# Optimization experiments

Hardware: AMD Instinct MI355X
Metric: run time of the kernel (lower is better)

The kernel has to match this reference:

```python
import jax, jax.numpy as jnp
import numpy as np

N = 50000
E = 1600000
R = 4
D_IN = 128
D_OUT = 128


def setup_inputs() -> dict:
    key = jax.random.key(0)
    ks = jax.random.split(key, 7)
    x = jax.random.normal(ks[0], (N, D_IN), dtype=jnp.float32)
    vals = jax.random.normal(ks[1], (R, E), dtype=jnp.float32) * (1.0 / 32.0)
    weight = jax.random.normal(ks[2], (D_IN, D_OUT), dtype=jnp.float32) * (1.0 / np.sqrt(D_IN))
    filt = jax.random.uniform(ks[3], (R * N, 1), dtype=jnp.float32, minval=0.9, maxval=1.1)
    bias = jnp.zeros((D_OUT,), dtype=jnp.float32)
    rows = jax.random.randint(ks[4], (R, E), 0, N, dtype=jnp.int32)
    cols = jax.random.randint(ks[5], (R, E), 0, N, dtype=jnp.int32)
    return {"x": x, "vals": vals, "weight": weight, "filt": filt,
            "bias": bias, "rows": rows, "cols": cols}


def _spmm(rows, cols, vals, h, n):
    # sparse [n,n] @ dense [n,d] via gather + segment_sum
    return jax.ops.segment_sum(vals[:, None] * h[cols], rows, num_segments=n)


def reference(x, vals, weight, filt, bias, rows, cols):
    n = x.shape[0]
    h = x @ weight                                    # [N, out]
    # cat(d_list, dim=0) @ h  ->  stack of D_i @ h, i.e. [R, N, out]
    y = jax.vmap(lambda r, c, v: _spmm(r, c, v, h, n))(rows, cols, vals)
    y = filt.reshape(rows.shape[0], n, 1) * y         # elementwise wavelet filter
    # cat(d_list, dim=1) @ y  ->  sum_i D_i @ y_i
    out = jax.vmap(lambda r, c, v, yy: _spmm(r, c, v, yy, n))(rows, cols, vals, y).sum(axis=0)
    return out + bias
```

## Files before the change

kernel.cpp:

```cpp
#include <hip/hip_runtime.h>

#define N_NODES 50000
#define N_EDGES 1600000
#define R_WAV 4
#define D 128
#define NB 391
#define CHUNK 4096
#define NPBLK ((N_EDGES + CHUNK - 1) / CHUNK)
#define MAXB 4800
#define RP_STRIDE 50016

typedef unsigned int u32;
typedef unsigned short u16;

static __device__ inline u16 f2bf(float f) {
    u32 u = __float_as_uint(f);
    u = (u + 0x7FFFu + ((u >> 16) & 1u)) >> 16;
    return (u16)u;
}
static __device__ inline float bf_lo(u32 u) { return __uint_as_float(u << 16); }
static __device__ inline float bf_hi(u32 u) { return __uint_as_float(u & 0xFFFF0000u); }

__global__ __launch_bounds__(128) void gemm_xw(const float* __restrict__ x,
                                               const float* __restrict__ W,
                                               u16* __restrict__ h) {
    const int j = threadIdx.x;
    const int row0 = blockIdx.x * 16;
    const float* xr = x + (size_t)row0 * D;
    float acc[16];
#pragma unroll
    for (int r = 0; r < 16; ++r) acc[r] = 0.f;
#pragma unroll 4
    for (int k = 0; k < 128; ++k) {
        const float w = W[k * D + j];
#pragma unroll
        for (int r = 0; r < 16; ++r) acc[r] += xr[r * D + k] * w;
    }
#pragma unroll
    for (int r = 0; r < 16; ++r) h[(size_t)(row0 + r) * D + j] = f2bf(acc[r]);
}

__global__ __launch_bounds__(256) void bucket_hist_all(const int* __restrict__ rows_all,
                                                       int* __restrict__ hist) {
    __shared__ int lh[NB];
    const int r = blockIdx.y;
    const int* rows = rows_all + (size_t)r * N_EDGES;
    const int tid = threadIdx.x;
    for (int i = tid; i < NB; i += 256) lh[i] = 0;
    __syncthreads();
    const int e0 = blockIdx.x * CHUNK;
    const int e1 = min(e0 + CHUNK, N_EDGES);
    for (int i = e0 + tid; i < e1; i += 256) atomicAdd(&lh[rows[i] >> 7], 1);
    __syncthreads();
    int* hc = hist + ((size_t)r * NPBLK + blockIdx.x) * NB;
    for (int i = tid; i < NB; i += 256) hc[i] = lh[i];
}

__global__ __launch_bounds__(512) void chunk_scan(const int* __restrict__ hist,
                                                  int* __restrict__ chunkpre,
                                                  int* __restrict__ cnt) {
    __shared__ int sa[512], sb[512];
    const int b = blockIdx.x;
    const int r = blockIdx.y;
    const int tid = threadIdx.x;
    const int v = (tid < NPBLK) ? hist[((size_t)r * NPBLK + tid) * NB + b] : 0;
    sa[tid] = v;
    int* cur = sa;
    int* nxt = sb;
    for (int d = 1; d < 512; d <<= 1) {
        __syncthreads();
        int t = cur[tid];
        if (tid >= d) t += cur[tid - d];
        nxt[tid] = t;
        int* tmp = cur; cur = nxt; nxt = tmp;
    }
    __syncthreads();
    const int excl = cur[tid] - v;
    if (tid < NPBLK) chunkpre[((size_t)r * NPBLK + tid) * NB + b] = excl;
    if (tid == NPBLK - 1) cnt[r * NB + b] = excl + v;
}

__global__ __launch_bounds__(512) void scan_buckets_all(const int* __restrict__ cnt4,
                                                        int* __restrict__ bptr4) {
    __shared__ int sa[512], sb[512];
    const int r = blockIdx.x;
    const int* cnt = cnt4 + r * NB;
    int* bptr = bptr4 + r * (NB + 1);
    const int tid = threadIdx.x;
    const int v = (tid < NB) ? cnt[tid] : 0;
    sa[tid] = v;
    int* cur = sa;
    int* nxt = sb;
    for (int d = 1; d < 512; d <<= 1) {
        __syncthreads();
        int t = cur[tid];
        if (tid >= d) t += cur[tid - d];
        nxt[tid] = t;
        int* tmp = cur; cur = nxt; nxt = tmp;
    }
    __syncthreads();
    const int excl = cur[tid] - v;
    if (tid <= NB) bptr[tid] = excl;
}

__global__ __launch_bounds__(256) void partition_kernel(const int* __restrict__ rows,
                                                        const int* __restrict__ cols,
                                                        const float* __restrict__ vals,
                                                        const int* __restrict__ bptr_all,
                                                        const int* __restrict__ chunkpre,
                                                        const int* __restrict__ hist,
                                                        u32* __restrict__ cvA,
                                                        u16* __restrict__ rowloc) {
    const int r = blockIdx.y;
    rows   += (size_t)r * N_EDGES;
    cols   += (size_t)r * N_EDGES;
    vals   += (size_t)r * N_EDGES;
    cvA    += (size_t)r * N_EDGES;
    rowloc += (size_t)r * N_EDGES;
    const int* bptr = bptr_all + r * (NB + 1);
    const int* hc   = hist     + ((size_t)r * NPBLK + blockIdx.x) * NB;
    const int* cp   = chunkpre + ((size_t)r * NPBLK + blockIdx.x) * NB;
    __shared__ int lh[NB], lptr[NB], lcur[NB], lbase[NB];
    __shared__ int sa[256], sb[256];
    __shared__ u32 st_cv[CHUNK];
    __shared__ u16 st_rl[CHUNK];
    const int tid = threadIdx.x;
    for (int i = tid; i < NB; i += 256) lh[i] = hc[i];
    __syncthreads();
    const int e0 = blockIdx.x * CHUNK;
    const int e1 = min(e0 + CHUNK, N_EDGES);
    const int cnt = e1 - e0;
    const int p0 = (2 * tid < NB) ? lh[2 * tid] : 0;
    const int p1 = (2 * tid + 1 < NB) ? lh[2 * tid + 1] : 0;
    sa[tid] = p0 + p1;
    int* cur = sa;
    int* nxt = sb;
    for (int d = 1; d < 256; d <<= 1) {
        __syncthreads();
        int t = cur[tid];
        if (tid >= d) t += cur[tid - d];
        nxt[tid] = t;
        int* tmp = cur; cur = nxt; nxt = tmp;
    }
    __syncthreads();
    const int pe = cur[tid] - (p0 + p1);
    if (2 * tid < NB)     { lptr[2 * tid] = pe;           lcur[2 * tid] = pe; }
    if (2 * tid + 1 < NB) { lptr[2 * tid + 1] = pe + p0;  lcur[2 * tid + 1] = pe + p0; }
    __syncthreads();
    for (int i = e0 + tid; i < e1; i += 256) {
        const int row = rows[i];
        const int b = row >> 7;
        const int pos = atomicAdd(&lcur[b], 1);
        st_cv[pos] = ((u32)f2bf(vals[i]) << 16) | ((u32)cols[i] & 0xFFFFu);
        st_rl[pos] = (u16)row;
    }
    for (int b = tid; b < NB; b += 256) lbase[b] = bptr[b] + cp[b] - lptr[b];
    __syncthreads();
    for (int i = tid; i < cnt; i += 256) {
        const u16 rl = st_rl[i];
        const int b = (int)rl >> 7;
        const int o = lbase[b] + i;
        cvA[o] = st_cv[i];
        rowloc[o] = rl;
    }
}

__global__ __launch_bounds__(256) void bucket_csr(const int* __restrict__ bptr_all,
                                                  const u32* __restrict__ cvA,
                                                  const u16* __restrict__ rowloc,
                                                  u32* __restrict__ cv4,
                                                  int* __restrict__ row_ptr) {
    const int r = blockIdx.y;
    const int* bptr = bptr_all + r * (NB + 1);
    cvA     += (size_t)r * N_EDGES;
    rowloc  += (size_t)r * N_EDGES;
    cv4     += (size_t)r * N_EDGES;
    row_ptr += r * RP_STRIDE;
    __shared__ int lh[128], lexcl[128], lcur[128];
    __shared__ u32 st[MAXB];
    const int b = blockIdx.x;
    const int s = bptr[b], e1 = bptr[b + 1];
    const int cnt = e1 - s;
    const int tid = threadIdx.x;
    if (tid < 128) lh[tid] = 0;
    __syncthreads();
    for (int i = s + tid; i < e1; i += 256)
        atomicAdd(&lh[(int)rowloc[i] & 127], 1);
    __syncthreads();
    if (tid < 64) {
        const int p0 = lh[2 * tid], p1 = lh[2 * tid + 1];
        int ssum = p0 + p1;
#pragma unroll
        for (int d = 1; d < 64; d <<= 1) {
            const int t = __shfl_up(ssum, d, 64);
            if (tid >= d) ssum += t;
        }
        const int pe = ssum - (p0 + p1);
        lexcl[2 * tid] = pe;          lcur[2 * tid] = pe;
        lexcl[2 * tid + 1] = pe + p0; lcur[2 * tid + 1] = pe + p0;
    }
    __syncthreads();
    for (int i = s + tid; i < e1; i += 256) {
        const int lr = (int)rowloc[i] & 127;
        const int pos = atomicAdd(&lcur[lr], 1);
        if (pos < MAXB) st[pos] = cvA[i];
    }
    __syncthreads();
    const int wb = (cnt < MAXB) ? cnt : MAXB;
    for (int i = tid; i < wb; i += 256) cv4[s + i] = st[i];
    if (tid < 128) {
        const int row = (b << 7) + tid;
        if (row < N_NODES) row_ptr[row] = s + lexcl[tid];
    }
    if (blockIdx.x == 0 && tid == 0) row_ptr[N_NODES] = N_EDGES;
}

__global__ __launch_bounds__(256) void spmm1(const int* __restrict__ row_ptr,
                                             const u32* __restrict__ cvp,
                                             const u32* __restrict__ h2,
                                             const float* __restrict__ filt,
                                             u32* __restrict__ y2) {
    const int r = blockIdx.y;
    row_ptr += r * RP_STRIDE;
    cvp     += (size_t)r * N_EDGES;
    filt    += (size_t)r * N_NODES;
    y2      += (size_t)r * (N_NODES * 64);
    const int row = __builtin_amdgcn_readfirstlane(blockIdx.x * 4 + (threadIdx.x >> 6));
    const int lane = threadIdx.x & 63;
    const int half = lane >> 5;
    const int l = lane & 31;
    int e = row_ptr[row];
    const int end = row_ptr[row + 1];
    float a0 = 0.f, a1 = 0.f, a2 = 0.f, a3 = 0.f;
    float b0 = 0.f, b1 = 0.f, b2 = 0.f, b3 = 0.f;
    for (; e + 16 <= end; e += 16) {
        u32 c[16];
#pragma unroll
        for (int i = 0; i < 16; ++i) c[i] = cvp[e + i];
        const u32 u0 = half ? c[1] : c[0];
        const u32 u1 = half ? c[3] : c[2];
        const u32 u2 = half ? c[5] : c[4];
        const u32 u3 = half ? c[7] : c[6];
        const u32 u4 = half ? c[9] : c[8];
        const u32 u5 = half ? c[11] : c[10];
        const u32 u6 = half ? c[13] : c[12];
        const u32 u7 = half ? c[15] : c[14];
        const uint2 g0 = *(const uint2*)(h2 + (u0 & 0xFFFFu) * 64 + 2 * l);
        const uint2 g1 = *(const uint2*)(h2 + (u1 & 0xFFFFu) * 64 + 2 * l);
        const uint2 g2 = *(const uint2*)(h2 + (u2 & 0xFFFFu) * 64 + 2 * l);
        const uint2 g3 = *(const uint2*)(h2 + (u3 & 0xFFFFu) * 64 + 2 * l);
        const uint2 g4 = *(const uint2*)(h2 + (u4 & 0xFFFFu) * 64 + 2 * l);
        const uint2 g5 = *(const uint2*)(h2 + (u5 & 0xFFFFu) * 64 + 2 * l);
        const uint2 g6 = *(const uint2*)(h2 + (u6 & 0xFFFFu) * 64 + 2 * l);
        const uint2 g7 = *(const uint2*)(h2 + (u7 & 0xFFFFu) * 64 + 2 * l);
        const float v0 = __uint_as_float(u0 & 0xFFFF0000u);
        const float v1 = __uint_as_float(u1 & 0xFFFF0000u);
        const float v2 = __uint_as_float(u2 & 0xFFFF0000u);
        const float v3 = __uint_as_float(u3 & 0xFFFF0000u);
        const float v4 = __uint_as_float(u4 & 0xFFFF0000u);
        const float v5 = __uint_as_float(u5 & 0xFFFF0000u);
        const float v6 = __uint_as_float(u6 & 0xFFFF0000u);
        const float v7 = __uint_as_float(u7 & 0xFFFF0000u);
        a0 += v0 * bf_lo(g0.x); a1 += v0 * bf_hi(g0.x);
        a2 += v0 * bf_lo(g0.y); a3 += v0 * bf_hi(g0.y);
        b0 += v1 * bf_lo(g1.x); b1 += v1 * bf_hi(g1.x);
        b2 += v1 * bf_lo(g1.y); b3 += v1 * bf_hi(g1.y);
        a0 += v2 * bf_lo(g2.x); a1 += v2 * bf_hi(g2.x);
        a2 += v2 * bf_lo(g2.y); a3 += v2 * bf_hi(g2.y);
        b0 += v3 * bf_lo(g3.x); b1 += v3 * bf_hi(g3.x);
        b2 += v3 * bf_lo(g3.y); b3 += v3 * bf_hi(g3.y);
        a0 += v4 * bf_lo(g4.x); a1 += v4 * bf_hi(g4.x);
        a2 += v4 * bf_lo(g4.y); a3 += v4 * bf_hi(g4.y);
        b0 += v5 * bf_lo(g5.x); b1 += v5 * bf_hi(g5.x);
        b2 += v5 * bf_lo(g5.y); b3 += v5 * bf_hi(g5.y);
        a0 += v6 * bf_lo(g6.x); a1 += v6 * bf_hi(g6.x);
        a2 += v6 * bf_lo(g6.y); a3 += v6 * bf_hi(g6.y);
        b0 += v7 * bf_lo(g7.x); b1 += v7 * bf_hi(g7.x);
        b2 += v7 * bf_lo(g7.y); b3 += v7 * bf_hi(g7.y);
    }
    for (; e + 8 <= end; e += 8) {
        const u32 c0 = cvp[e], c1 = cvp[e + 1], c2 = cvp[e + 2], c3 = cvp[e + 3];
        const u32 c4 = cvp[e + 4], c5 = cvp[e + 5], c6 = cvp[e + 6], c7 = cvp[e + 7];
        const u32 uA = half ? c1 : c0;
        const u32 uB = half ? c3 : c2;
        const u32 uC = half ? c5 : c4;
        const u32 uD = half ? c7 : c6;
        const uint2 gA = *(const uint2*)(h2 + (uA & 0xFFFFu) * 64 + 2 * l);
        const uint2 gB = *(const uint2*)(h2 + (uB & 0xFFFFu) * 64 + 2 * l);
        const uint2 gC = *(const uint2*)(h2 + (uC & 0xFFFFu) * 64 + 2 * l);
        const uint2 gD = *(const uint2*)(h2 + (uD & 0xFFFFu) * 64 + 2 * l);
        const float vA = __uint_as_float(uA & 0xFFFF0000u);
        const float vB = __uint_as_float(uB & 0xFFFF0000u);
        const float vC = __uint_as_float(uC & 0xFFFF0000u);
        const float vD = __uint_as_float(uD & 0xFFFF0000u);
        a0 += vA * bf_lo(gA.x); a1 += vA * bf_hi(gA.x);
        a2 += vA * bf_lo(gA.y); a3 += vA * bf_hi(gA.y);
        b0 += vB * bf_lo(gB.x); b1 += vB * bf_hi(gB.x);
        b2 += vB * bf_lo(gB.y); b3 += vB * bf_hi(gB.y);
        a0 += vC * bf_lo(gC.x); a1 += vC * bf_hi(gC.x);
        a2 += vC * bf_lo(gC.y); a3 += vC * bf_hi(gC.y);
        b0 += vD * bf_lo(gD.x); b1 += vD * bf_hi(gD.x);
        b2 += vD * bf_lo(gD.y); b3 += vD * bf_hi(gD.y);
    }
    for (; e < end; e += 2) {
        const u32 c0 = cvp[e];
        const u32 c1 = (e + 1 < end) ? cvp[e + 1] : 0u;
        const u32 uA = half ? c1 : c0;
        const uint2 gA = *(const uint2*)(h2 + (uA & 0xFFFFu) * 64 + 2 * l);
        const float vA = __uint_as_float(uA & 0xFFFF0000u);
        a0 += vA * bf_lo(gA.x); a1 += vA * bf_hi(gA.x);
        a2 += vA * bf_lo(gA.y); a3 += vA * bf_hi(gA.y);
    }
    a0 += b0; a1 += b1; a2 += b2; a3 += b3;
    a0 += __shfl_xor(a0, 32, 64);
    a1 += __shfl_xor(a1, 32, 64);
    a2 += __shfl_xor(a2, 32, 64);
    a3 += __shfl_xor(a3, 32, 64);
    const float f = filt[row];
    if (half == 0) {
        uint2 o;
        o.x = (u32)f2bf(f * a0) | ((u32)f2bf(f * a1) << 16);
        o.y = (u32)f2bf(f * a2) | ((u32)f2bf(f * a3) << 16);
        *(uint2*)(y2 + (size_t)row * 64 + 2 * l) = o;
    }
}

template <bool FIRST>
__global__ __launch_bounds__(256) void spmm2(const int* __restrict__ row_ptr,
                                             const u32* __restrict__ cvp,
                                             const u32* __restrict__ y2,
                                             const float* __restrict__ bias,
                                             float* __restrict__ out) {
    const int row = __builtin_amdgcn_readfirstlane(blockIdx.x * 4 + (threadIdx.x >> 6));
    const int lane = threadIdx.x & 63;
    const int half = lane >> 5;
    const int l = lane & 31;
    int e = row_ptr[row];
    const int end = row_ptr[row + 1];
    float a0 = 0.f, a1 = 0.f, a2 = 0.f, a3 = 0.f;
    float b0 = 0.f, b1 = 0.f, b2 = 0.f, b3 = 0.f;
    for (; e + 16 <= end; e += 16) {
        u32 c[16];
#pragma unroll
        for (int i = 0; i < 16; ++i) c[i] = cvp[e + i];
        const u32 u0 = half ? c[1] : c[0];
        const u32 u1 = half ? c[3] : c[2];
        const u32 u2 = half ? c[5] : c[4];
        const u32 u3 = half ? c[7] : c[6];
        const u32 u4 = half ? c[9] : c[8];
        const u32 u5 = half ? c[11] : c[10];
        const u32 u6 = half ? c[13] : c[12];
        const u32 u7 = half ? c[15] : c[14];
        const uint2 g0 = *(const uint2*)(y2 + (u0 & 0xFFFFu) * 64 + 2 * l);
        const uint2 g1 = *(const uint2*)(y2 + (u1 & 0xFFFFu) * 64 + 2 * l);
        const uint2 g2 = *(const uint2*)(y2 + (u2 & 0xFFFFu) * 64 + 2 * l);
        const uint2 g3 = *(const uint2*)(y2 + (u3 & 0xFFFFu) * 64 + 2 * l);
        const uint2 g4 = *(const uint2*)(y2 + (u4 & 0xFFFFu) * 64 + 2 * l);
        const uint2 g5 = *(const uint2*)(y2 + (u5 & 0xFFFFu) * 64 + 2 * l);
        const uint2 g6 = *(const uint2*)(y2 + (u6 & 0xFFFFu) * 64 + 2 * l);
        const uint2 g7 = *(const uint2*)(y2 + (u7 & 0xFFFFu) * 64 + 2 * l);
        const float v0 = __uint_as_float(u0 & 0xFFFF0000u);
        const float v1 = __uint_as_float(u1 & 0xFFFF0000u);
        const float v2 = __uint_as_float(u2 & 0xFFFF0000u);
        const float v3 = __uint_as_float(u3 & 0xFFFF0000u);
        const float v4 = __uint_as_float(u4 & 0xFFFF0000u);
        const float v5 = __uint_as_float(u5 & 0xFFFF0000u);
        const float v6 = __uint_as_float(u6 & 0xFFFF0000u);
        const float v7 = __uint_as_float(u7 & 0xFFFF0000u);
        a0 += v0 * bf_lo(g0.x); a1 += v0 * bf_hi(g0.x);
        a2 += v0 * bf_lo(g0.y); a3 += v0 * bf_hi(g0.y);
        b0 += v1 * bf_lo(g1.x); b1 += v1 * bf_hi(g1.x);
        b2 += v1 * bf_lo(g1.y); b3 += v1 * bf_hi(g1.y);
        a0 += v2 * bf_lo(g2.x); a1 += v2 * bf_hi(g2.x);
        a2 += v2 * bf_lo(g2.y); a3 += v2 * bf_hi(g2.y);
        b0 += v3 * bf_lo(g3.x); b1 += v3 * bf_hi(g3.x);
        b2 += v3 * bf_lo(g3.y); b3 += v3 * bf_hi(g3.y);
        a0 += v4 * bf_lo(g4.x); a1 += v4 * bf_hi(g4.x);
        a2 += v4 * bf_lo(g4.y); a3 += v4 * bf_hi(g4.y);
        b0 += v5 * bf_lo(g5.x); b1 += v5 * bf_hi(g5.x);
        b2 += v5 * bf_lo(g5.y); b3 += v5 * bf_hi(g5.y);
        a0 += v6 * bf_lo(g6.x); a1 += v6 * bf_hi(g6.x);
        a2 += v6 * bf_lo(g6.y); a3 += v6 * bf_hi(g6.y);
        b0 += v7 * bf_lo(g7.x); b1 += v7 * bf_hi(g7.x);
        b2 += v7 * bf_lo(g7.y); b3 += v7 * bf_hi(g7.y);
    }
    for (; e + 8 <= end; e += 8) {
        const u32 c0 = cvp[e], c1 = cvp[e + 1], c2 = cvp[e + 2], c3 = cvp[e + 3];
        const u32 c4 = cvp[e + 4], c5 = cvp[e + 5], c6 = cvp[e + 6], c7 = cvp[e + 7];
        const u32 uA = half ? c1 : c0;
        const u32 uB = half ? c3 : c2;
        const u32 uC = half ? c5 : c4;
        const u32 uD = half ? c7 : c6;
        const uint2 gA = *(const uint2*)(y2 + (uA & 0xFFFFu) * 64 + 2 * l);
        const uint2 gB = *(const uint2*)(y2 + (uB & 0xFFFFu) * 64 + 2 * l);
        const uint2 gC = *(const uint2*)(y2 + (uC & 0xFFFFu) * 64 + 2 * l);
        const uint2 gD = *(const uint2*)(y2 + (uD & 0xFFFFu) * 64 + 2 * l);
        const float vA = __uint_as_float(uA & 0xFFFF0000u);
        const float vB = __uint_as_float(uB & 0xFFFF0000u);
        const float vC = __uint_as_float(uC & 0xFFFF0000u);
        const float vD = __uint_as_float(uD & 0xFFFF0000u);
        a0 += vA * bf_lo(gA.x); a1 += vA * bf_hi(gA.x);
        a2 += vA * bf_lo(gA.y); a3 += vA * bf_hi(gA.y);
        b0 += vB * bf_lo(gB.x); b1 += vB * bf_hi(gB.x);
        b2 += vB * bf_lo(gB.y); b3 += vB * bf_hi(gB.y);
        a0 += vC * bf_lo(gC.x); a1 += vC * bf_hi(gC.x);
        a2 += vC * bf_lo(gC.y); a3 += vC * bf_hi(gC.y);
        b0 += vD * bf_lo(gD.x); b1 += vD * bf_hi(gD.x);
        b2 += vD * bf_lo(gD.y); b3 += vD * bf_hi(gD.y);
    }
    for (; e < end; e += 2) {
        const u32 c0 = cvp[e];
        const u32 c1 = (e + 1 < end) ? cvp[e + 1] : 0u;
        const u32 uA = half ? c1 : c0;
        const uint2 gA = *(const uint2*)(y2 + (uA & 0xFFFFu) * 64 + 2 * l);
        const float vA = __uint_as_float(uA & 0xFFFF0000u);
        a0 += vA * bf_lo(gA.x); a1 += vA * bf_hi(gA.x);
        a2 += vA * bf_lo(gA.y); a3 += vA * bf_hi(gA.y);
    }
    a0 += b0; a1 += b1; a2 += b2; a3 += b3;
    a0 += __shfl_xor(a0, 32, 64);
    a1 += __shfl_xor(a1, 32, 64);
    a2 += __shfl_xor(a2, 32, 64);
    a3 += __shfl_xor(a3, 32, 64);
    if (half == 0) {
        float* op = out + (size_t)row * D + 4 * l;
        if (FIRST) {
            const float4 bb = *(const float4*)(bias + 4 * l);
            *(float4*)op = make_float4(a0 + bb.x, a1 + bb.y, a2 + bb.z, a3 + bb.w);
        } else {
            const float4 cc = *(const float4*)op;
            *(float4*)op = make_float4(cc.x + a0, cc.y + a1, cc.z + a2, cc.w + a3);
        }
    }
}

extern "C" void kernel_launch(void* const* d_in, const int* in_sizes, int n_in,
                              void* d_out, int out_size, void* d_ws, size_t ws_size,
                              hipStream_t stream) {
    const float* x    = (const float*)d_in[0];
    const float* vals = (const float*)d_in[1];
    const float* W    = (const float*)d_in[2];
    const float* filt = (const float*)d_in[3];
    const float* bias = (const float*)d_in[4];
    const int*   rows = (const int*)d_in[5];
    const int*   cols = (const int*)d_in[6];
    float* out = (float*)d_out;

    char* ws = (char*)d_ws;
    u16*  h      = (u16*)(ws);
    u32*  cvA    = (u32*)(ws + 12800000);
    u16*  rowloc = (u16*)(ws + 38400000);
    u32*  y2     = (u32*)(ws + 12800000);
    u32*  cv4    = (u32*)(ws + 64000000);
    int*  hist   = (int*)(ws + 64000000);
    int*  cpre   = (int*)(ws + 66446096);
    int*  rp     = (int*)(ws + 89600000);
    int*  cnt4   = (int*)(ws + 90400512);
    int*  bptr4  = (int*)(ws + 90406768);

    bucket_hist_all<<<dim3(NPBLK, R_WAV), 256, 0, stream>>>(rows, hist);
    chunk_scan<<<dim3(NB, R_WAV), 512, 0, stream>>>(hist, cpre, cnt4);
    scan_buckets_all<<<R_WAV, 512, 0, stream>>>(cnt4, bptr4);
    partition_kernel<<<dim3(NPBLK, R_WAV), 256, 0, stream>>>(rows, cols, vals,
                                                             bptr4, cpre, hist,
                                                             cvA, rowloc);
    bucket_csr<<<dim3(NB, R_WAV), 256, 0, stream>>>(bptr4, cvA, rowloc, cv4, rp);

    gemm_xw<<<N_NODES / 16, 128, 0, stream>>>(x, W, h);

    spmm1<<<dim3(N_NODES / 4, R_WAV), 256, 0, stream>>>(rp, cv4, (const u32*)h,
                                                        filt, y2);
    for (int r = 0; r < R_WAV; ++r) {
        const int* rp_r  = rp + r * RP_STRIDE;
        const u32* cv4_r = cv4 + (size_t)r * N_EDGES;
        const u32* y2_r  = y2 + (size_t)r * (N_NODES * 64);
        if (r == 0)
            spmm2<true><<<N_NODES / 4, 256, 0, stream>>>(rp_r, cv4_r, y2_r, bias, out);
        else
            spmm2<false><<<N_NODES / 4, 256, 0, stream>>>(rp_r, cv4_r, y2_r, bias, out);
    }
}
```

Baseline: 683.1 us.

## Split SpMM feature dimension into two column phases to shrink gather working set

Both SpMM kernels now process the 128-wide feature dimension in two separate launches, each handling 64 columns (32 packed bf16 pairs) per row. Each gather fetches 4 bytes per lane instead of 8, so the set of rows touched in one pass is half as many bytes and is more likely to stay in L2/MALL. The cost is that the CSR index/value stream is read twice, launch count doubles, and the per-gather request is narrower.

```diff
diff --git a/kernel.cpp b/kernel.cpp
--- a/kernel.cpp
+++ b/kernel.cpp
@@ -219,20 +219,22 @@
                                              const u32* __restrict__ cvp,
                                              const u32* __restrict__ h2,
                                              const float* __restrict__ filt,
-                                             u32* __restrict__ y2) {
+                                             u32* __restrict__ y2,
+                                             int ph) {
     const int r = blockIdx.y;
     row_ptr += r * RP_STRIDE;
     cvp     += (size_t)r * N_EDGES;
     filt    += (size_t)r * N_NODES;
     y2      += (size_t)r * (N_NODES * 64);
+    const u32* hb = h2 + ph * 32;
     const int row = __builtin_amdgcn_readfirstlane(blockIdx.x * 4 + (threadIdx.x >> 6));
     const int lane = threadIdx.x & 63;
     const int half = lane >> 5;
     const int l = lane & 31;
     int e = row_ptr[row];
     const int end = row_ptr[row + 1];
-    float a0 = 0.f, a1 = 0.f, a2 = 0.f, a3 = 0.f;
-    float b0 = 0.f, b1 = 0.f, b2 = 0.f, b3 = 0.f;
+    float a0 = 0.f, a1 = 0.f;
+    float b0 = 0.f, b1 = 0.f;
     for (; e + 16 <= end; e += 16) {
         u32 c[16];
 #pragma unroll
@@ -245,14 +247,14 @@
         const u32 u5 = half ? c[11] : c[10];
         const u32 u6 = half ? c[13] : c[12];
         const u32 u7 = half ? c[15] : c[14];
-        const uint2 g0 = *(const uint2*)(h2 + (u0 & 0xFFFFu) * 64 + 2 * l);
-        const uint2 g1 = *(const uint2*)(h2 + (u1 & 0xFFFFu) * 64 + 2 * l);
-        const uint2 g2 = *(const uint2*)(h2 + (u2 & 0xFFFFu) * 64 + 2 * l);
-        const uint2 g3 = *(const uint2*)(h2 + (u3 & 0xFFFFu) * 64 + 2 * l);
-        const uint2 g4 = *(const uint2*)(h2 + (u4 & 0xFFFFu) * 64 + 2 * l);
-        const uint2 g5 = *(const uint2*)(h2 + (u5 & 0xFFFFu) * 64 + 2 * l);
-        const uint2 g6 = *(const uint2*)(h2 + (u6 & 0xFFFFu) * 64 + 2 * l);
-        const uint2 g7 = *(const uint2*)(h2 + (u7 & 0xFFFFu) * 64 + 2 * l);
+        const u32 g0 = hb[(u0 & 0xFFFFu) * 64 + l];
+        const u32 g1 = hb[(u1 & 0xFFFFu) * 64 + l];
+        const u32 g2 = hb[(u2 & 0xFFFFu) * 64 + l];
+        const u32 g3 = hb[(u3 & 0xFFFFu) * 64 + l];
+        const u32 g4 = hb[(u4 & 0xFFFFu) * 64 + l];
+        const u32 g5 = hb[(u5 & 0xFFFFu) * 64 + l];
+        const u32 g6 = hb[(u6 & 0xFFFFu) * 64 + l];
+        const u32 g7 = hb[(u7 & 0xFFFFu) * 64 + l];
         const float v0 = __uint_as_float(u0 & 0xFFFF0000u);
         const float v1 = __uint_as_float(u1 & 0xFFFF0000u);
         const float v2 = __uint_as_float(u2 & 0xFFFF0000u);
@@ -261,22 +263,14 @@
         const float v5 = __uint_as_float(u5 & 0xFFFF0000u);
         const float v6 = __uint_as_float(u6 & 0xFFFF0000u);
         const float v7 = __uint_as_float(u7 & 0xFFFF0000u);
-        a0 += v0 * bf_lo(g0.x); a1 += v0 * bf_hi(g0.x);
-        a2 += v0 * bf_lo(g0.y); a3 += v0 * bf_hi(g0.y);
-        b0 += v1 * bf_lo(g1.x); b1 += v1 * bf_hi(g1.x);
-        b2 += v1 * bf_lo(g1.y); b3 += v1 * bf_hi(g1.y);
-        a0 += v2 * bf_lo(g2.x); a1 += v2 * bf_hi(g2.x);
-        a2 += v2 * bf_lo(g2.y); a3 += v2 * bf_hi(g2.y);
-        b0 += v3 * bf_lo(g3.x); b1 += v3 * bf_hi(g3.x);
-        b2 += v3 * bf_lo(g3.y); b3 += v3 * bf_hi(g3.y);
-        a0 += v4 * bf_lo(g4.x); a1 += v4 * bf_hi(g4.x);
-        a2 += v4 * bf_lo(g4.y); a3 += v4 * bf_hi(g4.y);
-        b0 += v5 * bf_lo(g5.x); b1 += v5 * bf_hi(g5.x);
-        b2 += v5 * bf_lo(g5.y); b3 += v5 * bf_hi(g5.y);
-        a0 += v6 * bf_lo(g6.x); a1 += v6 * bf_hi(g6.x);
-        a2 += v6 * bf_lo(g6.y); a3 += v6 * bf_hi(g6.y);
-        b0 += v7 * bf_lo(g7.x); b1 += v7 * bf_hi(g7.x);
-        b2 += v7 * bf_lo(g7.y); b3 += v7 * bf_hi(g7.y);
+        a0 += v0 * bf_lo(g0); a1 += v0 * bf_hi(g0);
+        b0 += v1 * bf_lo(g1); b1 += v1 * bf_hi(g1);
+        a0 += v2 * bf_lo(g2); a1 += v2 * bf_hi(g2);
+        b0 += v3 * bf_lo(g3); b1 += v3 * bf_hi(g3);
+        a0 += v4 * bf_lo(g4); a1 += v4 * bf_hi(g4);
+        b0 += v5 * bf_lo(g5); b1 += v5 * bf_hi(g5);
+        a0 += v6 * bf_lo(g6); a1 += v6 * bf_hi(g6);
+        b0 += v7 * bf_lo(g7); b1 += v7 * bf_hi(g7);
     }
     for (; e + 8 <= end; e += 8) {
         const u32 c0 = cvp[e], c1 = cvp[e + 1], c2 = cvp[e + 2], c3 = cvp[e + 3];
@@ -285,43 +279,34 @@
         const u32 uB = half ? c3 : c2;
         const u32 uC = half ? c5 : c4;
         const u32 uD = half ? c7 : c6;
-        const uint2 gA = *(const uint2*)(h2 + (uA & 0xFFFFu) * 64 + 2 * l);
-        const uint2 gB = *(const uint2*)(h2 + (uB & 0xFFFFu) * 64 + 2 * l);
-        const uint2 gC = *(const uint2*)(h2 + (uC & 0xFFFFu) * 64 + 2 * l);
-        const uint2 gD = *(const uint2*)(h2 + (uD & 0xFFFFu) * 64 + 2 * l);
+        const u32 gA = hb[(uA & 0xFFFFu) * 64 + l];
+        const u32 gB = hb[(uB & 0xFFFFu) * 64 + l];
+        const u32 gC = hb[(uC & 0xFFFFu) * 64 + l];
+        const u32 gD = hb[(uD & 0xFFFFu) * 64 + l];
         const float vA = __uint_as_float(uA & 0xFFFF0000u);
         const float vB = __uint_as_float(uB & 0xFFFF0000u);
         const float vC = __uint_as_float(uC & 0xFFFF0000u);
         const float vD = __uint_as_float(uD & 0xFFFF0000u);
-        a0 += vA * bf_lo(gA.x); a1 += vA * bf_hi(gA.x);
-        a2 += vA * bf_lo(gA.y); a3 += vA * bf_hi(gA.y);
-        b0 += vB * bf_lo(gB.x); b1 += vB * bf_hi(gB.x);
-        b2 += vB * bf_lo(gB.y); b3 += vB * bf_hi(gB.y);
-        a0 += vC * bf_lo(gC.x); a1 += vC * bf_hi(gC.x);
-        a2 += vC * bf_lo(gC.y); a3 += vC * bf_hi(gC.y);
-        b0 += vD * bf_lo(gD.x); b1 += vD * bf_hi(gD.x);
-        b2 += vD * bf_lo(gD.y); b3 += vD * bf_hi(gD.y);
+        a0 += vA * bf_lo(gA); a1 += vA * bf_hi(gA);
+        b0 += vB * bf_lo(gB); b1 += vB * bf_hi(gB);
+        a0 += vC * bf_lo(gC); a1 += vC * bf_hi(gC);
+        b0 += vD * bf_lo(gD); b1 += vD * bf_hi(gD);
     }
     for (; e < end; e += 2) {
         const u32 c0 = cvp[e];
         const u32 c1 = (e + 1 < end) ? cvp[e + 1] : 0u;
         const u32 uA = half ? c1 : c0;
-        const uint2 gA = *(const uint2*)(h2 + (uA & 0xFFFFu) * 64 + 2 * l);
+        const u32 gA = hb[(uA & 0xFFFFu) * 64 + l];
         const float vA = __uint_as_float(uA & 0xFFFF0000u);
-        a0 += vA * bf_lo(gA.x); a1 += vA * bf_hi(gA.x);
-        a2 += vA * bf_lo(gA.y); a3 += vA * bf_hi(gA.y);
-    }
-    a0 += b0; a1 += b1; a2 += b2; a3 += b3;
+        a0 += vA * bf_lo(gA); a1 += vA * bf_hi(gA);
+    }
+    a0 += b0; a1 += b1;
     a0 += __shfl_xor(a0, 32, 64);
     a1 += __shfl_xor(a1, 32, 64);
-    a2 += __shfl_xor(a2, 32, 64);
-    a3 += __shfl_xor(a3, 32, 64);
     const float f = filt[row];
     if (half == 0) {
-        uint2 o;
-        o.x = (u32)f2bf(f * a0) | ((u32)f2bf(f * a1) << 16);
-        o.y = (u32)f2bf(f * a2) | ((u32)f2bf(f * a3) << 16);
-        *(uint2*)(y2 + (size_t)row * 64 + 2 * l) = o;
+        const u32 o = (u32)f2bf(f * a0) | ((u32)f2bf(f * a1) << 16);
+        y2[(size_t)row * 64 + ph * 32 + l] = o;
     }
 }
 
@@ -330,15 +315,17 @@
                                              const u32* __restrict__ cvp,
                                              const u32* __restrict__ y2,
                                              const float* __restrict__ bias,
-                                             float* __restrict__ out) {
+                                             float* __restrict__ out,
+                                             int ph) {
+    const u32* yb = y2 + ph * 32;
     const int row = __builtin_amdgcn_readfirstlane(blockIdx.x * 4 + (threadIdx.x >> 6));
     const int lane = threadIdx.x & 63;
     const int half = lane >> 5;
     const int l = lane & 31;
     int e = row_ptr[row];
     const int end = row_ptr[row + 1];
-    float a0 = 0.f, a1 = 0.f, a2 = 0.f, a3 = 0.f;
-    float b0 = 0.f, b1 = 0.f, b2 = 0.f, b3 = 0.f;
+    float a0 = 0.f, a1 = 0.f;
+    float b0 = 0.f, b1 = 0.f;
     for (; e + 16 <= end; e += 16) {
         u32 c[16];
 #pragma unroll
@@ -351,14 +338,14 @@
         const u32 u5 = half ? c[11] : c[10];
         const u32 u6 = half ? c[13] : c[12];
         const u32 u7 = half ? c[15] : c[14];
-        const uint2 g0 = *(const uint2*)(y2 + (u0 & 0xFFFFu) * 64 + 2 * l);
-        const uint2 g1 = *(const uint2*)(y2 + (u1 & 0xFFFFu) * 64 + 2 * l);
-        const uint2 g2 = *(const uint2*)(y2 + (u2 & 0xFFFFu) * 64 + 2 * l);
-        const uint2 g3 = *(const uint2*)(y2 + (u3 & 0xFFFFu) * 64 + 2 * l);
-        const uint2 g4 = *(const uint2*)(y2 + (u4 & 0xFFFFu) * 64 + 2 * l);
-        const uint2 g5 = *(const uint2*)(y2 + (u5 & 0xFFFFu) * 64 + 2 * l);
-        const uint2 g6 = *(const uint2*)(y2 + (u6 & 0xFFFFu) * 64 + 2 * l);
-        const uint2 g7 = *(const uint2*)(y2 + (u7 & 0xFFFFu) * 64 + 2 * l);
+        const u32 g0 = yb[(u0 & 0xFFFFu) * 64 + l];
+        const u32 g1 = yb[(u1 & 0xFFFFu) * 64 + l];
+        const u32 g2 = yb[(u2 & 0xFFFFu) * 64 + l];
+        const u32 g3 = yb[(u3 & 0xFFFFu) * 64 + l];
+        const u32 g4 = yb[(u4 & 0xFFFFu) * 64 + l];
+        const u32 g5 = yb[(u5 & 0xFFFFu) * 64 + l];
+        const u32 g6 = yb[(u6 & 0xFFFFu) * 64 + l];
+        const u32 g7 = yb[(u7 & 0xFFFFu) * 64 + l];
         const float v0 = __uint_as_float(u0 & 0xFFFF0000u);
         const float v1 = __uint_as_float(u1 & 0xFFFF0000u);
         const float v2 = __uint_as_float(u2 & 0xFFFF0000u);
@@ -367,22 +354,14 @@
         const float v5 = __uint_as_float(u5 & 0xFFFF0000u);
         const float v6 = __uint_as_float(u6 & 0xFFFF0000u);
         const float v7 = __uint_as_float(u7 & 0xFFFF0000u);
-        a0 += v0 * bf_lo(g0.x); a1 += v0 * bf_hi(g0.x);
-        a2 += v0 * bf_lo(g0.y); a3 += v0 * bf_hi(g0.y);
-        b0 += v1 * bf_lo(g1.x); b1 += v1 * bf_hi(g1.x);
-        b2 += v1 * bf_lo(g1.y); b3 += v1 * bf_hi(g1.y);
-        a0 += v2 * bf_lo(g2.x); a1 += v2 * bf_hi(g2.x);
-        a2 += v2 * bf_lo(g2.y); a3 += v2 * bf_hi(g2.y);
-        b0 += v3 * bf_lo(g3.x); b1 += v3 * bf_hi(g3.x);
-        b2 += v3 * bf_lo(g3.y); b3 += v3 * bf_hi(g3.y);
-        a0 += v4 * bf_lo(g4.x); a1 += v4 * bf_hi(g4.x);
-        a2 += v4 * bf_lo(g4.y); a3 += v4 * bf_hi(g4.y);
-        b0 += v5 * bf_lo(g5.x); b1 += v5 * bf_hi(g5.x);
-        b2 += v5 * bf_lo(g5.y); b3 += v5 * bf_hi(g5.y);
-        a0 += v6 * bf_lo(g6.x); a1 += v6 * bf_hi(g6.x);
-        a2 += v6 * bf_lo(g6.y); a3 += v6 * bf_hi(g6.y);
-        b0 += v7 * bf_lo(g7.x); b1 += v7 * bf_hi(g7.x);
-        b2 += v7 * bf_lo(g7.y); b3 += v7 * bf_hi(g7.y);
+        a0 += v0 * bf_lo(g0); a1 += v0 * bf_hi(g0);
+        b0 += v1 * bf_lo(g1); b1 += v1 * bf_hi(g1);
+        a0 += v2 * bf_lo(g2); a1 += v2 * bf_hi(g2);
+        b0 += v3 * bf_lo(g3); b1 += v3 * bf_hi(g3);
+        a0 += v4 * bf_lo(g4); a1 += v4 * bf_hi(g4);
+        b0 += v5 * bf_lo(g5); b1 += v5 * bf_hi(g5);
+        a0 += v6 * bf_lo(g6); a1 += v6 * bf_hi(g6);
+        b0 += v7 * bf_lo(g7); b1 += v7 * bf_hi(g7);
     }
     for (; e + 8 <= end; e += 8) {
         const u32 c0 = cvp[e], c1 = cvp[e + 1], c2 = cvp[e + 2], c3 = cvp[e + 3];
@@ -391,45 +370,40 @@
         const u32 uB = half ? c3 : c2;
         const u32 uC = half ? c5 : c4;
         const u32 uD = half ? c7 : c6;
-        const uint2 gA = *(const uint2*)(y2 + (uA & 0xFFFFu) * 64 + 2 * l);
-        const uint2 gB = *(const uint2*)(y2 + (uB & 0xFFFFu) * 64 + 2 * l);
-        const uint2 gC = *(const uint2*)(y2 + (uC & 0xFFFFu) * 64 + 2 * l);
-        const uint2 gD = *(const uint2*)(y2 + (uD & 0xFFFFu) * 64 + 2 * l);
+        const u32 gA = yb[(uA & 0xFFFFu) * 64 + l];
+        const u32 gB = yb[(uB & 0xFFFFu) * 64 + l];
+        const u32 gC = yb[(uC & 0xFFFFu) * 64 + l];
+        const u32 gD = yb[(uD & 0xFFFFu) * 64 + l];
         const float vA = __uint_as_float(uA & 0xFFFF0000u);
         const float vB = __uint_as_float(uB & 0xFFFF0000u);
         const float vC = __uint_as_float(uC & 0xFFFF0000u);
         const float vD = __uint_as_float(uD & 0xFFFF0000u);
-        a0 += vA * bf_lo(gA.x); a1 += vA * bf_hi(gA.x);
-        a2 += vA * bf_lo(gA.y); a3 += vA * bf_hi(gA.y);
-        b0 += vB * bf_lo(gB.x); b1 += vB * bf_hi(gB.x);
-        b2 += vB * bf_lo(gB.y); b3 += vB * bf_hi(gB.y);
-        a0 += vC * bf_lo(gC.x); a1 += vC * bf_hi(gC.x);
-        a2 += vC * bf_lo(gC.y); a3 += vC * bf_hi(gC.y);
-        b0 += vD * bf_lo(gD.x); b1 += vD * bf_hi(gD.x);
-        b2 += vD * bf_lo(gD.y); b3 += vD * bf_hi(gD.y);
+        a0 += vA * bf_lo(gA); a1 += vA * bf_hi(gA);
+        b0 += vB * bf_lo(gB); b1 += vB * bf_hi(gB);
+        a0 += vC * bf_lo(gC); a1 += vC * bf_hi(gC);
+        b0 += vD * bf_lo(gD); b1 += vD * bf_hi(gD);
     }
     for (; e < end; e += 2) {
         const u32 c0 = cvp[e];
         const u32 c1 = (e + 1 < end) ? cvp[e + 1] : 0u;
         const u32 uA = half ? c1 : c0;
-        const uint2 gA = *(const uint2*)(y2 + (uA & 0xFFFFu) * 64 + 2 * l);
+        const u32 gA = yb[(uA & 0xFFFFu) * 64 + l];
         const float vA = __uint_as_float(uA & 0xFFFF0000u);
-        a0 += vA * bf_lo(gA.x); a1 += vA * bf_hi(gA.x);
-        a2 += vA * bf_lo(gA.y); a3 += vA * bf_hi(gA.y);
-    }
-    a0 += b0; a1 += b1; a2 += b2; a3 += b3;
+        a0 += vA * bf_lo(gA); a1 += vA * bf_hi(gA);
+    }
+    a0 += b0; a1 += b1;
     a0 += __shfl_xor(a0, 32, 64);
     a1 += __shfl_xor(a1, 32, 64);
-    a2 += __shfl_xor(a2, 32, 64);
-    a3 += __shfl_xor(a3, 32, 64);
     if (half == 0) {
-        float* op = out + (size_t)row * D + 4 * l;
+        float* op = out + (size_t)row * D + ph * 64 + 2 * l;
         if (FIRST) {
-            const float4 bb = *(const float4*)(bias + 4 * l);
-            *(float4*)op = make_float4(a0 + bb.x, a1 + bb.y, a2 + bb.z, a3 + bb.w);
+            const float2 bb = *(const float2*)(bias + ph * 64 + 2 * l);
+            const float2 o = make_float2(a0 + bb.x, a1 + bb.y);
+            *(float2*)op = o;
         } else {
-            const float4 cc = *(const float4*)op;
-            *(float4*)op = make_float4(cc.x + a0, cc.y + a1, cc.z + a2, cc.w + a3);
+            const float2 cc = *(const float2*)op;
+            const float2 o = make_float2(cc.x + a0, cc.y + a1);
+            *(float2*)op = o;
         }
     }
 }
@@ -468,15 +442,20 @@
 
     gemm_xw<<<N_NODES / 16, 128, 0, stream>>>(x, W, h);
 
-    spmm1<<<dim3(N_NODES / 4, R_WAV), 256, 0, stream>>>(rp, cv4, (const u32*)h,
-                                                        filt, y2);
+    for (int ph = 0; ph < 2; ++ph)
+        spmm1<<<dim3(N_NODES / 4, R_WAV), 256, 0, stream>>>(rp, cv4, (const u32*)h,
+                                                            filt, y2, ph);
     for (int r = 0; r < R_WAV; ++r) {
         const int* rp_r  = rp + r * RP_STRIDE;
         const u32* cv4_r = cv4 + (size_t)r * N_EDGES;
         const u32* y2_r  = y2 + (size_t)r * (N_NODES * 64);
-        if (r == 0)
-            spmm2<true><<<N_NODES / 4, 256, 0, stream>>>(rp_r, cv4_r, y2_r, bias, out);
-        else
-            spmm2<false><<<N_NODES / 4, 256, 0, stream>>>(rp_r, cv4_r, y2_r, bias, out);
-    }
-}
+        for (int ph = 0; ph < 2; ++ph) {
+            if (r == 0)
+                spmm2<true><<<N_NODES / 4, 256, 0, stream>>>(rp_r, cv4_r, y2_r,
+                                                             bias, out, ph);
+            else
+                spmm2<false><<<N_NODES / 4, 256, 0, stream>>>(rp_r, cv4_r, y2_r,
+                                                              bias, out, ph);
+        }
+    }
+}
```

Result: slower. 732.3 us (+7.2%).
